# Optimization experiments

Measured on AMD Instinct MI355X. Metric: run time of the kernel, lower is better.

## Reference

```python
import jax, jax.numpy as jnp
import numpy as np

N = 100000        # total nodes across the batch of graphs
E = 1600000       # directed edges (avg degree 16)
B = 64            # number of graphs
IN_C = 4
HID = 128


def gcn_conv(x, W, b, src, dst, n):
    """PyG GCNConv: add self-loops, symmetric deg normalization, scatter-add."""
    h = x @ W                                   # [n, out]
    loop = jnp.arange(n)
    s = jnp.concatenate([src, loop])            # [E+n] sources (with self-loops)
    d = jnp.concatenate([dst, loop])            # [E+n] targets
    deg = jax.ops.segment_sum(jnp.ones_like(s, dtype=h.dtype), d, num_segments=n)
    dinv = jnp.where(deg > 0, jax.lax.rsqrt(deg), 0.0)
    norm = dinv[s] * dinv[d]                    # [E+n]
    out = jax.ops.segment_sum(h[s] * norm[:, None], d, num_segments=n)
    return out + b


def setup_inputs() -> dict:
    key = jax.random.key(0)
    k1, k2, k3, k4, k5, k6, k7 = jax.random.split(key, 7)
    x = jax.random.normal(k1, (N, IN_C), dtype=jnp.float32)
    edge_index = jax.random.randint(k2, (2, E), 0, N, dtype=jnp.int64)
    batch = jnp.sort(jax.random.randint(k3, (N,), 0, B, dtype=jnp.int64))
    W1 = jax.random.normal(k4, (IN_C, HID), dtype=jnp.float32) / np.sqrt(IN_C)
    b1 = jnp.zeros((HID,), dtype=jnp.float32)
    W2 = jax.random.normal(k5, (HID, HID), dtype=jnp.float32) / np.sqrt(HID)
    b2 = jnp.zeros((HID,), dtype=jnp.float32)
    return {"x": x, "edge_index": edge_index, "batch": batch,
            "W1": W1, "b1": b1, "W2": W2, "b2": b2}


def reference(x, edge_index, batch, W1, b1, W2, b2):
    src, dst = edge_index[0], edge_index[1]
    n = x.shape[0]
    h = jax.nn.relu(gcn_conv(x, W1, b1, src, dst, n))
    h = jax.nn.relu(gcn_conv(h, W2, b2, src, dst, n))
    # global_mean_pool: scatter-mean by graph id
    s = jax.ops.segment_sum(h, batch, num_segments=B)                       # [B, HID]
    cnt = jax.ops.segment_sum(jnp.ones((n,), h.dtype), batch, num_segments=B)
    return s / jnp.maximum(cnt, 1.0)[:, None]
```

## Files before the change

kernel.cpp:

```cpp
#include <hip/hip_runtime.h>

#define TPB 256
#define HID 128
#define IN_C 4
#define SLOT_C 32

typedef __attribute__((ext_vector_type(8))) short bf16x8;
typedef __attribute__((ext_vector_type(4))) float f32x4;

union FragU { uint4 u; bf16x8 b; };

__device__ __forceinline__ unsigned f2bf(float f) {
    unsigned u = __float_as_uint(f);
    return (u + 0x7fffu + ((u >> 16) & 1u)) >> 16;
}
__device__ __forceinline__ float bf_lo(unsigned u) { return __uint_as_float(u << 16); }
__device__ __forceinline__ float bf_hi(unsigned u) { return __uint_as_float(u & 0xffff0000u); }

__global__ void k_prep(int* cursor, float* out, int n, int outsz,
                       const float* __restrict__ W2, unsigned short* w2f,
                       const int* __restrict__ batch, int* cnt, int bg,
                       int* ovf_cnt) {
    int nbA = (n + TPB - 1) / TPB;
    int b = blockIdx.x;
    if (b < nbA) {
        int i = b * TPB + threadIdx.x;
        if (i < n) cursor[i] = 0;
        if (i < outsz) out[i] = 0.0f;
    } else if (b < nbA + 64) {
        int i = (b - nbA) * TPB + threadIdx.x;
        if (i < HID * HID) {
            int j = i & 7, frag = i >> 3;
            int lane = frag & 63, blk = frag >> 6;
            int kk = blk >> 3, nt = blk & 7;
            int quad = lane >> 4, nloc = lane & 15;
            int k = kk * 32 + quad * 8 + j;
            int c = nt * 16 + nloc;
            w2f[i] = (unsigned short)f2bf(W2[k * HID + c]);
        }
    } else {
        int g = threadIdx.x;
        if (g == 0) *ovf_cnt = 0;
        if (g < bg) {
            int lo0 = 0, hi0 = n;
            while (lo0 < hi0) { int m = (lo0 + hi0) >> 1; if (batch[m] < g) lo0 = m + 1; else hi0 = m; }
            int lo1 = lo0, hi1 = n;
            while (lo1 < hi1) { int m = (lo1 + hi1) >> 1; if (batch[m] < g + 1) lo1 = m + 1; else hi1 = m; }
            cnt[g] = lo1 - lo0;
        }
    }
}

__global__ void k_bucket(const int* __restrict__ src, const int* __restrict__ dst,
                         int* cursor, int* slots, int* ovf, int* ovf_cnt,
                         int e, int n) {
    int pass = blockIdx.x & 7;
    int i = (blockIdx.x >> 3) * blockDim.x + threadIdx.x;
    if (i >= e) return;
    int rlo = (int)(((long)n * pass) >> 3);
    int rhi = (int)(((long)n * (pass + 1)) >> 3);
    int d = dst[i];
    if (d >= rlo && d < rhi) {
        int p = atomicAdd(&cursor[d], 1);
        if (p < SLOT_C) {
            slots[d * SLOT_C + p] = src[i];
        } else {
            int o = atomicAdd(ovf_cnt, 1);
            ovf[2 * o] = src[i];
            ovf[2 * o + 1] = d;
        }
    }
}

__global__ void k_dinv(const int* __restrict__ cursor, float* dinv, int n) {
    int i = blockIdx.x * blockDim.x + threadIdx.x;
    if (i < n) dinv[i] = rsqrtf((float)cursor[i] + 1.0f);
}

__global__ __launch_bounds__(256) void k_g1f1(
        const int* __restrict__ cursor, const int* __restrict__ slots,
        const int* __restrict__ ovf, const int* __restrict__ ovf_cnt,
        const float* __restrict__ dinv, const float* __restrict__ x,
        const float* __restrict__ W1, const float* __restrict__ b1,
        unsigned* f1p, int n) {
    __shared__ float xs[256 * 5];
    int t = threadIdx.x;
    int v0 = blockIdx.x * 256;

    int v = v0 + t;
    if (v < n) {
        float dv = dinv[v];
        const float4* x4 = (const float4*)x;
        float4 xv = x4[v];
        float sl = dv * dv;
        float4 A = make_float4(sl * xv.x, sl * xv.y, sl * xv.z, sl * xv.w);
        float4 B = make_float4(0.f, 0.f, 0.f, 0.f);
        float4 C = make_float4(0.f, 0.f, 0.f, 0.f);
        float4 D = make_float4(0.f, 0.f, 0.f, 0.f);
        int deg = cursor[v];
        int m = deg < SLOT_C ? deg : SLOT_C;
        const int* sb = slots + v * SLOT_C;
        int e = 0;
        for (; e + 4 <= m; e += 4) {
            int s0 = sb[e], s1 = sb[e + 1], s2 = sb[e + 2], s3 = sb[e + 3];
            float n0 = dinv[s0] * dv, n1 = dinv[s1] * dv;
            float n2 = dinv[s2] * dv, n3 = dinv[s3] * dv;
            float4 r0 = x4[s0], r1 = x4[s1], r2 = x4[s2], r3 = x4[s3];
            A.x = fmaf(n0, r0.x, A.x); A.y = fmaf(n0, r0.y, A.y);
            A.z = fmaf(n0, r0.z, A.z); A.w = fmaf(n0, r0.w, A.w);
            B.x = fmaf(n1, r1.x, B.x); B.y = fmaf(n1, r1.y, B.y);
            B.z = fmaf(n1, r1.z, B.z); B.w = fmaf(n1, r1.w, B.w);
            C.x = fmaf(n2, r2.x, C.x); C.y = fmaf(n2, r2.y, C.y);
            C.z = fmaf(n2, r2.z, C.z); C.w = fmaf(n2, r2.w, C.w);
            D.x = fmaf(n3, r3.x, D.x); D.y = fmaf(n3, r3.y, D.y);
            D.z = fmaf(n3, r3.z, D.z); D.w = fmaf(n3, r3.w, D.w);
        }
        for (; e < m; e++) {
            int s = sb[e];
            float nm = dinv[s] * dv;
            float4 r = x4[s];
            A.x = fmaf(nm, r.x, A.x); A.y = fmaf(nm, r.y, A.y);
            A.z = fmaf(nm, r.z, A.z); A.w = fmaf(nm, r.w, A.w);
        }
        if (deg > SLOT_C) {
            int oc = *ovf_cnt;
            for (int k = 0; k < oc; k++) {
                if (ovf[2 * k + 1] == v) {
                    int s = ovf[2 * k];
                    float nm = dinv[s] * dv;
                    float4 r = x4[s];
                    A.x = fmaf(nm, r.x, A.x); A.y = fmaf(nm, r.y, A.y);
                    A.z = fmaf(nm, r.z, A.z); A.w = fmaf(nm, r.w, A.w);
                }
            }
        }
        xs[t * 5 + 0] = (A.x + B.x) + (C.x + D.x);
        xs[t * 5 + 1] = (A.y + B.y) + (C.y + D.y);
        xs[t * 5 + 2] = (A.z + B.z) + (C.z + D.z);
        xs[t * 5 + 3] = (A.w + B.w) + (C.w + D.w);
    }
    __syncthreads();

    int cp = t & 63;
    int c0 = cp * 2, c1 = c0 + 1;
    float w00 = W1[c0],           w01 = W1[c1];
    float w10 = W1[HID + c0],     w11 = W1[HID + c1];
    float w20 = W1[2 * HID + c0], w21 = W1[2 * HID + c1];
    float w30 = W1[3 * HID + c0], w31 = W1[3 * HID + c1];
    float bb0 = b1[c0],           bb1 = b1[c1];
    int g = t >> 6;
    for (int iter = 0; iter < 64; iter++) {
        int node = iter * 4 + g;
        int vv = v0 + node;
        if (vv >= n) break;
        float x0 = xs[node * 5 + 0], x1 = xs[node * 5 + 1];
        float x2 = xs[node * 5 + 2], x3 = xs[node * 5 + 3];
        float s0 = fmaf(x0, w00, fmaf(x1, w10, fmaf(x2, w20, fmaf(x3, w30, bb0))));
        float s1 = fmaf(x0, w01, fmaf(x1, w11, fmaf(x2, w21, fmaf(x3, w31, bb1))));
        s0 = s0 > 0.0f ? s0 : 0.0f;
        s1 = s1 > 0.0f ? s1 : 0.0f;
        f1p[(size_t)vv * 64 + cp] = f2bf(s0) | (f2bf(s1) << 16);
    }
}

__global__ __launch_bounds__(256) void k_gather2(
        const int* __restrict__ cursor, const int* __restrict__ slots,
        const int* __restrict__ ovf, const int* __restrict__ ovf_cnt,
        const float* __restrict__ dinv, const unsigned* __restrict__ f1p,
        unsigned* acc2b, int n) {
    int wv = threadIdx.x >> 6;
    int ln = threadIdx.x & 63;
    int h  = ln >> 5;
    int q  = ln & 31;
    int v = blockIdx.x * 4 + wv;
    if (v >= n) return;
    float dv = dinv[v];
    const uint2* F = (const uint2*)f1p;

    uint2 us = F[(size_t)v * 32 + q];
    float sl = (h == 0) ? dv * dv : 0.0f;
    float A[4] = { sl * bf_lo(us.x), sl * bf_hi(us.x),
                   sl * bf_lo(us.y), sl * bf_hi(us.y) };
    float B[4] = {0.f, 0.f, 0.f, 0.f};
    float C[4] = {0.f, 0.f, 0.f, 0.f};
    float D[4] = {0.f, 0.f, 0.f, 0.f};

    int deg = cursor[v];
    int m = deg < SLOT_C ? deg : SLOT_C;
    const int* sb = slots + v * SLOT_C;
    int e = 0;
    for (; e + 8 <= m; e += 8) {
        int sA = sb[e + h];
        int sB = sb[e + 2 + h];
        int sC = sb[e + 4 + h];
        int sD = sb[e + 6 + h];
        float nA = dinv[sA] * dv, nB = dinv[sB] * dv;
        float nC = dinv[sC] * dv, nD = dinv[sD] * dv;
        uint2 uA = F[(size_t)sA * 32 + q];
        uint2 uB = F[(size_t)sB * 32 + q];
        uint2 uC = F[(size_t)sC * 32 + q];
        uint2 uD = F[(size_t)sD * 32 + q];
        A[0] = fmaf(nA, bf_lo(uA.x), A[0]); A[1] = fmaf(nA, bf_hi(uA.x), A[1]);
        A[2] = fmaf(nA, bf_lo(uA.y), A[2]); A[3] = fmaf(nA, bf_hi(uA.y), A[3]);
        B[0] = fmaf(nB, bf_lo(uB.x), B[0]); B[1] = fmaf(nB, bf_hi(uB.x), B[1]);
        B[2] = fmaf(nB, bf_lo(uB.y), B[2]); B[3] = fmaf(nB, bf_hi(uB.y), B[3]);
        C[0] = fmaf(nC, bf_lo(uC.x), C[0]); C[1] = fmaf(nC, bf_hi(uC.x), C[1]);
        C[2] = fmaf(nC, bf_lo(uC.y), C[2]); C[3] = fmaf(nC, bf_hi(uC.y), C[3]);
        D[0] = fmaf(nD, bf_lo(uD.x), D[0]); D[1] = fmaf(nD, bf_hi(uD.x), D[1]);
        D[2] = fmaf(nD, bf_lo(uD.y), D[2]); D[3] = fmaf(nD, bf_hi(uD.y), D[3]);
    }
    for (; e + 2 <= m; e += 2) {
        int s = sb[e + h];
        float nm = dinv[s] * dv;
        uint2 u = F[(size_t)s * 32 + q];
        A[0] = fmaf(nm, bf_lo(u.x), A[0]); A[1] = fmaf(nm, bf_hi(u.x), A[1]);
        A[2] = fmaf(nm, bf_lo(u.y), A[2]); A[3] = fmaf(nm, bf_hi(u.y), A[3]);
    }
    if (e < m) {
        int s = sb[e];
        float nm = (h == 0) ? dinv[s] * dv : 0.0f;
        uint2 u = F[(size_t)s * 32 + q];
        A[0] = fmaf(nm, bf_lo(u.x), A[0]); A[1] = fmaf(nm, bf_hi(u.x), A[1]);
        A[2] = fmaf(nm, bf_lo(u.y), A[2]); A[3] = fmaf(nm, bf_hi(u.y), A[3]);
    }
    if (deg > SLOT_C) {
        int oc = *ovf_cnt;
        for (int k = 0; k < oc; k++) {
            if (ovf[2 * k + 1] == v && h == 0) {
                int s = ovf[2 * k];
                float nm = dinv[s] * dv;
                uint2 u = F[(size_t)s * 32 + q];
                A[0] = fmaf(nm, bf_lo(u.x), A[0]); A[1] = fmaf(nm, bf_hi(u.x), A[1]);
                A[2] = fmaf(nm, bf_lo(u.y), A[2]); A[3] = fmaf(nm, bf_hi(u.y), A[3]);
            }
        }
    }

    float o0 = (A[0] + B[0]) + (C[0] + D[0]);
    float o1 = (A[1] + B[1]) + (C[1] + D[1]);
    float o2 = (A[2] + B[2]) + (C[2] + D[2]);
    float o3 = (A[3] + B[3]) + (C[3] + D[3]);
    o0 += __shfl_xor(o0, 32, 64);
    o1 += __shfl_xor(o1, 32, 64);
    o2 += __shfl_xor(o2, 32, 64);
    o3 += __shfl_xor(o3, 32, 64);
    if (h == 0) {
        uint2 w;
        w.x = f2bf(o0) | (f2bf(o1) << 16);
        w.y = f2bf(o2) | (f2bf(o3) << 16);
        ((uint2*)acc2b)[(size_t)v * 32 + q] = w;
    }
}

__global__ __launch_bounds__(256) void k_mm2_pool(
        const unsigned* __restrict__ acc2b, const unsigned short* __restrict__ w2f,
        const float* __restrict__ b2, const int* __restrict__ batch,
        float* out, int n) {
    __shared__ int bch[64];
    int t = threadIdx.x;
    int w = t >> 6, lane = t & 63;
    int quad = lane >> 4, nloc = lane & 15;
    int v0 = blockIdx.x * 64;
    if (t < 64) {
        int v = v0 + t;
        bch[t] = (v < n) ? batch[v] : -1;
    }
    __syncthreads();

    int va = v0 + w * 16 + nloc;
    if (va >= n) va = n - 1;

    const uint4* A4 = (const uint4*)acc2b;
    const uint4* B4 = (const uint4*)w2f;

    f32x4 acc[8];
#pragma unroll
    for (int nt = 0; nt < 8; nt++) acc[nt] = (f32x4){0.f, 0.f, 0.f, 0.f};

#pragma unroll
    for (int kk = 0; kk < 4; kk++) {
        FragU af;
        af.u = A4[(size_t)va * 16 + kk * 4 + quad];
#pragma unroll
        for (int nt = 0; nt < 8; nt++) {
            FragU bf;
            bf.u = B4[(kk * 8 + nt) * 64 + lane];
            acc[nt] = __builtin_amdgcn_mfma_f32_16x16x32_bf16(af.b, bf.b, acc[nt], 0, 0, 0);
        }
    }

    int b0 = bch[w * 16], b15 = bch[w * 16 + 15];
    if (b0 == b15 && b0 >= 0) {
#pragma unroll
        for (int nt = 0; nt < 8; nt++) {
            float bias = b2[nt * 16 + nloc];
            float s = 0.f;
#pragma unroll
            for (int reg = 0; reg < 4; reg++) {
                float f = acc[nt][reg] + bias;
                s += f > 0.f ? f : 0.f;
            }
            s += __shfl_xor(s, 16, 64);
            s += __shfl_xor(s, 32, 64);
            if (lane < 16) atomicAdd(&out[b0 * HID + nt * 16 + lane], s);
        }
    } else {
#pragma unroll
        for (int nt = 0; nt < 8; nt++) {
            float bias = b2[nt * 16 + nloc];
            int cur = -1; float run = 0.f;
#pragma unroll
            for (int reg = 0; reg < 4; reg++) {
                int b = bch[w * 16 + quad * 4 + reg];
                if (b < 0) continue;
                float f = acc[nt][reg] + bias;
                f = f > 0.f ? f : 0.f;
                if (b != cur) {
                    if (cur >= 0) atomicAdd(&out[cur * HID + nt * 16 + nloc], run);
                    run = 0.f; cur = b;
                }
                run += f;
            }
            if (cur >= 0) atomicAdd(&out[cur * HID + nt * 16 + nloc], run);
        }
    }
}

__global__ void k_div(float* out, const int* __restrict__ cnt, int outsz) {
    int i = blockIdx.x * blockDim.x + threadIdx.x;
    if (i < outsz) {
        int b = i >> 7;
        float cf = (float)cnt[b];
        out[i] = out[i] / fmaxf(cf, 1.0f);
    }
}

extern "C" void kernel_launch(void* const* d_in, const int* in_sizes, int n_in,
                              void* d_out, int out_size, void* d_ws, size_t ws_size,
                              hipStream_t stream) {
    const float* x   = (const float*)d_in[0];
    const int* ei    = (const int*)d_in[1];
    const int* batch = (const int*)d_in[2];
    const float* W1  = (const float*)d_in[3];
    const float* b1  = (const float*)d_in[4];
    const float* W2  = (const float*)d_in[5];
    const float* b2  = (const float*)d_in[6];
    float* out = (float*)d_out;

    int n  = in_sizes[0] / IN_C;
    int e  = in_sizes[1] / 2;
    int bg = out_size / HID;
    const int* src = ei;
    const int* dst = ei + e;

    size_t off_b = 0;
    char* base = (char*)d_ws;
    auto carve = [&](size_t bytes) -> void* {
        void* p = base + off_b;
        off_b += (bytes + 255) & ~(size_t)255;
        return p;
    };
    int*            cursor  = (int*)carve((size_t)n * 4);
    int*            slots   = (int*)carve((size_t)n * SLOT_C * 4);
    int*            ovf     = (int*)carve((size_t)e * 2 * 4);
    int*            ovf_cnt = (int*)carve(256);
    float*          dinv    = (float*)carve((size_t)n * 4);
    unsigned*       f1p     = (unsigned*)carve((size_t)n * 64 * 4);
    unsigned*       acc2b   = (unsigned*)carve((size_t)n * 64 * 4);
    unsigned short* w2f     = (unsigned short*)carve((size_t)HID * HID * 2);
    int*            cnt     = (int*)carve((size_t)bg * 4);
    (void)ws_size;

    int gN = (n + TPB - 1) / TPB;
    int gE = (e + TPB - 1) / TPB;

    k_prep<<<gN + 64 + 1, TPB, 0, stream>>>(cursor, out, n, out_size, W2, w2f,
                                            batch, cnt, bg, ovf_cnt);
    k_bucket<<<gE * 8, TPB, 0, stream>>>(src, dst, cursor, slots, ovf, ovf_cnt, e, n);
    k_dinv<<<gN, TPB, 0, stream>>>(cursor, dinv, n);
    k_g1f1<<<gN, TPB, 0, stream>>>(cursor, slots, ovf, ovf_cnt, dinv, x, W1, b1, f1p, n);
    k_gather2<<<(n + 3) / 4, 256, 0, stream>>>(cursor, slots, ovf, ovf_cnt, dinv, f1p, acc2b, n);
    k_mm2_pool<<<(n + 63) / 64, 256, 0, stream>>>(acc2b, w2f, b2, batch, out, n);
    k_div<<<(out_size + TPB - 1) / TPB, TPB, 0, stream>>>(out, cnt, out_size);
}
```

Baseline: 274.3 us.

## Partition edges by destination range before bucketing into CSR slots

```diff
diff --git a/kernel.cpp b/kernel.cpp
--- a/kernel.cpp
+++ b/kernel.cpp
@@ -4,6 +4,8 @@
 #define HID 128
 #define IN_C 4
 #define SLOT_C 32
+#define NPART 8
+#define OVF_CAP 131072
 
 typedef __attribute__((ext_vector_type(8))) short bf16x8;
 typedef __attribute__((ext_vector_type(4))) float f32x4;
@@ -20,7 +22,7 @@
 __global__ void k_prep(int* cursor, float* out, int n, int outsz,
                        const float* __restrict__ W2, unsigned short* w2f,
                        const int* __restrict__ batch, int* cnt, int bg,
-                       int* ovf_cnt) {
+                       int* ovf_cnt, int* pcur) {
     int nbA = (n + TPB - 1) / TPB;
     int b = blockIdx.x;
     if (b < nbA) {
@@ -41,6 +43,7 @@
     } else {
         int g = threadIdx.x;
         if (g == 0) *ovf_cnt = 0;
+        if (g >= 64 && g < 64 + NPART) pcur[g - 64] = 0;
         if (g < bg) {
             int lo0 = 0, hi0 = n;
             while (lo0 < hi0) { int m = (lo0 + hi0) >> 1; if (batch[m] < g) lo0 = m + 1; else hi0 = m; }
@@ -51,23 +54,47 @@
     }
 }
 
-__global__ void k_bucket(const int* __restrict__ src, const int* __restrict__ dst,
-                         int* cursor, int* slots, int* ovf, int* ovf_cnt,
-                         int e, int n) {
-    int pass = blockIdx.x & 7;
-    int i = (blockIdx.x >> 3) * blockDim.x + threadIdx.x;
-    if (i >= e) return;
-    int rlo = (int)(((long)n * pass) >> 3);
-    int rhi = (int)(((long)n * (pass + 1)) >> 3);
-    int d = dst[i];
-    if (d >= rlo && d < rhi) {
-        int p = atomicAdd(&cursor[d], 1);
-        if (p < SLOT_C) {
-            slots[d * SLOT_C + p] = src[i];
-        } else {
-            int o = atomicAdd(ovf_cnt, 1);
-            ovf[2 * o] = src[i];
-            ovf[2 * o + 1] = d;
+__global__ __launch_bounds__(256) void k_part(
+        const int* __restrict__ src, const int* __restrict__ dst,
+        int2* elist, int* pcur, int e, int n, int cap) {
+    __shared__ int lcnt[NPART];
+    __shared__ int lbase[NPART];
+    int t = threadIdx.x;
+    int i = blockIdx.x * blockDim.x + t;
+    if (t < NPART) lcnt[t] = 0;
+    __syncthreads();
+    int s = 0, d = 0, p = -1, r = 0;
+    if (i < e) {
+        s = src[i];
+        d = dst[i];
+        p = (int)(((long long)d * NPART) / n);
+        r = atomicAdd(&lcnt[p], 1);
+    }
+    __syncthreads();
+    if (t < NPART && lcnt[t] > 0) lbase[t] = atomicAdd(&pcur[t], lcnt[t]);
+    __syncthreads();
+    if (i < e) {
+        int idx = lbase[p] + r;
+        if (idx < cap)
+            elist[(size_t)p * cap + idx] = make_int2(s, d);
+    }
+}
+
+__global__ __launch_bounds__(256) void k_build(
+        const int2* __restrict__ elist, const int* __restrict__ pcur,
+        int* cursor, int* slots, int* ovf, int* ovf_cnt, int cap) {
+    int p = blockIdx.x & (NPART - 1);
+    int j = (blockIdx.x >> 3) * blockDim.x + threadIdx.x;
+    if (j >= pcur[p]) return;
+    int2 ed = elist[(size_t)p * cap + j];
+    int pos = atomicAdd(&cursor[ed.y], 1);
+    if (pos < SLOT_C) {
+        slots[ed.y * SLOT_C + pos] = ed.x;
+    } else {
+        int o = atomicAdd(ovf_cnt, 1);
+        if (o < OVF_CAP) {
+            ovf[2 * o] = ed.x;
+            ovf[2 * o + 1] = ed.y;
         }
     }
 }
@@ -360,10 +387,13 @@
         off_b += (bytes + 255) & ~(size_t)255;
         return p;
     };
+    int cap = e / NPART + 4096;
     int*            cursor  = (int*)carve((size_t)n * 4);
     int*            slots   = (int*)carve((size_t)n * SLOT_C * 4);
-    int*            ovf     = (int*)carve((size_t)e * 2 * 4);
+    int*            ovf     = (int*)carve((size_t)OVF_CAP * 2 * 4);
     int*            ovf_cnt = (int*)carve(256);
+    int*            pcur    = (int*)carve(256);
+    int2*           elist   = (int2*)carve((size_t)NPART * cap * 8);
     float*          dinv    = (float*)carve((size_t)n * 4);
     unsigned*       f1p     = (unsigned*)carve((size_t)n * 64 * 4);
     unsigned*       acc2b   = (unsigned*)carve((size_t)n * 64 * 4);
@@ -373,10 +403,12 @@
 
     int gN = (n + TPB - 1) / TPB;
     int gE = (e + TPB - 1) / TPB;
+    int gB = ((cap + TPB - 1) / TPB) * NPART;
 
     k_prep<<<gN + 64 + 1, TPB, 0, stream>>>(cursor, out, n, out_size, W2, w2f,
-                                            batch, cnt, bg, ovf_cnt);
-    k_bucket<<<gE * 8, TPB, 0, stream>>>(src, dst, cursor, slots, ovf, ovf_cnt, e, n);
+                                            batch, cnt, bg, ovf_cnt, pcur);
+    k_part<<<gE, TPB, 0, stream>>>(src, dst, elist, pcur, e, n, cap);
+    k_build<<<gB, TPB, 0, stream>>>(elist, pcur, cursor, slots, ovf, ovf_cnt, cap);
     k_dinv<<<gN, TPB, 0, stream>>>(cursor, dinv, n);
     k_g1f1<<<gN, TPB, 0, stream>>>(cursor, slots, ovf, ovf_cnt, dinv, x, W1, b1, f1p, n);
     k_gather2<<<(n + 3) / 4, 256, 0, stream>>>(cursor, slots, ovf, ovf_cnt, dinv, f1p, acc2b, n);
```

New measurement: 344.5 us. +25.6%, slower.
